# Performance work log

Measured on AMD Instinct MI355X. Metric: run time of the kernel, lower is better.

The kernel has to match this reference:

```python
import jax, jax.numpy as jnp
import numpy as np

B, H = 1024, 256
HP = H // 2  # hyperparams_dim
W_SCALE = 0.08  # kaiming-uniform-like magnitude to keep tanh unsaturated


def setup_inputs() -> dict:
    key = jax.random.key(0)
    ks = jax.random.split(key, 8)
    return {
        "h_0": jax.random.normal(ks[0], (B, 1, H), dtype=jnp.float32),
        "h_t": jax.random.normal(ks[1], (B, 1, H), dtype=jnp.float32),
        "msg": jax.random.normal(ks[2], (B, 1, H), dtype=jnp.float32),
        "c": jax.random.uniform(ks[3], (1,), dtype=jnp.float32),
        "fc1_w": jax.random.normal(ks[4], (HP, H), dtype=jnp.float32) * W_SCALE,
        "fc2_w": jax.random.normal(ks[5], (HP, HP), dtype=jnp.float32) * W_SCALE,
        "fc3_w": jax.random.normal(ks[6], (HP, HP), dtype=jnp.float32) * W_SCALE,
        "fc4_w": jax.random.normal(ks[7], (2 * H * H, HP), dtype=jnp.float32) * W_SCALE,
    }


def reference(h_0, h_t, msg, c, fc1_w, fc2_w, fc3_w, fc4_w):
    # torch code clamps self.c into [0, 1] before use
    cc = jnp.clip(c, 0.0, 1.0)
    h = cc * h_0 + (1.0 - cc) * h_t                     # [B, 1, H]
    x = jnp.tanh(jnp.einsum('bsh,ph->bsp', h, fc1_w))    # [B, 1, HP]
    x = jnp.tanh(jnp.einsum('bsp,qp->bsq', x, fc2_w))    # [B, 1, HP]
    x = jnp.tanh(jnp.einsum('bsq,rq->bsr', x, fc3_w))    # [B, 1, HP]
    f4 = jnp.einsum('bsr,wr->bsw', x, fc4_w)             # [B, 1, 2*H*H]
    g1 = f4[..., : H * H].reshape(-1, H, H)              # [B, H, H]
    g2 = f4[..., H * H :].reshape(-1, H, H)              # [B, H, H]
    # F.linear(msg[i], g) == msg[i] @ g.T, batched over B
    g1_out = jnp.tanh(jnp.einsum('bsh,bkh->bsk', msg, g1))  # [B, 1, H]
    out = jnp.einsum('bsk,bok->bso', g1_out, g2)             # [B, 1, H]
    return out
```

## Files before the change

kernel.cpp:

```cpp
#include <hip/hip_runtime.h>
#include <hip/hip_bf16.h>

#define HDIM 256
#define HPDIM 128

typedef short bf8 __attribute__((ext_vector_type(8)));
typedef float f32x4 __attribute__((ext_vector_type(4)));

__device__ inline unsigned pkbf2(float a, float b) {
  float2 f; f.x = a; f.y = b;
  __hip_bfloat162 h = __float22bfloat162_rn(f);
  unsigned u; __builtin_memcpy(&u, &h, 4); return u;
}
__device__ inline unsigned short bfbits(float v) {
  __hip_bfloat16 h = __float2bfloat16(v);
  unsigned short u; __builtin_memcpy(&u, &h, 2); return u;
}
__device__ inline uint4 pack8u(float4 a, float4 b) {
  uint4 r;
  r.x = pkbf2(a.x, a.y); r.y = pkbf2(a.z, a.w);
  r.z = pkbf2(b.x, b.y); r.w = pkbf2(b.z, b.w);
  return r;
}
__device__ inline float fast_tanh(float x) {
  float t = __expf(2.0f * x);
  return 1.0f - 2.0f * __builtin_amdgcn_rcpf(t + 1.0f);
}
__device__ inline bf8 wfrag(const float* __restrict__ s) {
  float4 a = *(const float4*)s, b = *(const float4*)(s + 4);
  uint4 u = pack8u(a, b);
  bf8 r; __builtin_memcpy(&r, &u, 16); return r;
}

__global__ __launch_bounds__(256) void k_prep(
    const float* __restrict__ h0, const float* __restrict__ htv,
    const float* __restrict__ cp,
    const float* __restrict__ w1, const float* __restrict__ w2,
    const float* __restrict__ w3, const float* __restrict__ msg,
    short* __restrict__ x3f, float* __restrict__ msgTT) {
  const int t = threadIdx.x;
  const int bx = blockIdx.x;

  if (bx >= 64) {
    const int b0 = (bx - 64) * 64;
    #pragma unroll
    for (int it = 0; it < 16; ++it) {
      int u = it * 256 + t;
      int bl = u & 63, g = u >> 6;
      float4 v = *(const float4*)(msg + (size_t)(b0 + bl) * HDIM + g * 4);
      *(float4*)(msgTT + (size_t)g * 4096 + (b0 + bl) * 4) = v;
    }
    return;
  }

  __shared__ char hbuf[8192];
  __shared__ char xa[4096];
  __shared__ char xb[4096];
  const int wave = t >> 6, lane = t & 63;
  const int r16 = lane & 15, quad = lane >> 4;
  const int b0 = bx * 16;
  const float cc = fminf(fmaxf(cp[0], 0.f), 1.f);

  #pragma unroll
  for (int it = 0; it < 2; ++it) {
    int flat = it * 2048 + t * 8;
    int row = flat >> 8, col = flat & 255, kb = col >> 3;
    int gi = (b0 + row) * HDIM + col;
    float4 a = *(const float4*)(h0 + gi);
    float4 b = *(const float4*)(htv + gi);
    float4 va, vb;
    va.x = cc*a.x + (1.f-cc)*b.x; va.y = cc*a.y + (1.f-cc)*b.y;
    va.z = cc*a.z + (1.f-cc)*b.z; va.w = cc*a.w + (1.f-cc)*b.w;
    a = *(const float4*)(h0 + gi + 4); b = *(const float4*)(htv + gi + 4);
    vb.x = cc*a.x + (1.f-cc)*b.x; vb.y = cc*a.y + (1.f-cc)*b.y;
    vb.z = cc*a.z + (1.f-cc)*b.z; vb.w = cc*a.w + (1.f-cc)*b.w;
    *(uint4*)(hbuf + row*512 + ((kb ^ (row & 7)) << 4)) = pack8u(va, vb);
  }
  __syncthreads();

  {
    f32x4 acc[2] = {};
    #pragma unroll
    for (int ks = 0; ks < 8; ++ks) {
      bf8 af = *(bf8*)(hbuf + r16*512 + (((ks*4 + quad) ^ (r16 & 7)) << 4));
      #pragma unroll
      for (int nt = 0; nt < 2; ++nt) {
        bf8 bw_ = wfrag(w1 + ((wave*2 + nt)*16 + r16) * 256 + ks*32 + quad*8);
        acc[nt] = __builtin_amdgcn_mfma_f32_16x16x32_bf16(af, bw_, acc[nt], 0, 0, 0);
      }
    }
    #pragma unroll
    for (int nt = 0; nt < 2; ++nt)
      #pragma unroll
      for (int i = 0; i < 4; ++i) {
        int row = quad*4 + i, col = wave*32 + nt*16 + r16;
        *(unsigned short*)(xa + row*256 + (((col >> 3) ^ (row & 7)) << 4) + ((col & 7) << 1))
            = bfbits(fast_tanh(acc[nt][i]));
      }
  }
  __syncthreads();
  {
    f32x4 acc[2] = {};
    #pragma unroll
    for (int ks = 0; ks < 4; ++ks) {
      bf8 af = *(bf8*)(xa + r16*256 + (((ks*4 + quad) ^ (r16 & 7)) << 4));
      #pragma unroll
      for (int nt = 0; nt < 2; ++nt) {
        bf8 bw_ = wfrag(w2 + ((wave*2 + nt)*16 + r16) * 128 + ks*32 + quad*8);
        acc[nt] = __builtin_amdgcn_mfma_f32_16x16x32_bf16(af, bw_, acc[nt], 0, 0, 0);
      }
    }
    #pragma unroll
    for (int nt = 0; nt < 2; ++nt)
      #pragma unroll
      for (int i = 0; i < 4; ++i) {
        int row = quad*4 + i, col = wave*32 + nt*16 + r16;
        *(unsigned short*)(xb + row*256 + (((col >> 3) ^ (row & 7)) << 4) + ((col & 7) << 1))
            = bfbits(fast_tanh(acc[nt][i]));
      }
  }
  __syncthreads();
  {
    f32x4 acc[2] = {};
    #pragma unroll
    for (int ks = 0; ks < 4; ++ks) {
      bf8 af = *(bf8*)(xb + r16*256 + (((ks*4 + quad) ^ (r16 & 7)) << 4));
      #pragma unroll
      for (int nt = 0; nt < 2; ++nt) {
        bf8 bw_ = wfrag(w3 + ((wave*2 + nt)*16 + r16) * 128 + ks*32 + quad*8);
        acc[nt] = __builtin_amdgcn_mfma_f32_16x16x32_bf16(af, bw_, acc[nt], 0, 0, 0);
      }
    }
    #pragma unroll
    for (int nt = 0; nt < 2; ++nt)
      #pragma unroll
      for (int i = 0; i < 4; ++i) {
        int row = quad*4 + i, col = wave*32 + nt*16 + r16;
        *(unsigned short*)(xa + row*256 + (((col >> 3) ^ (row & 7)) << 4) + ((col & 7) << 1))
            = bfbits(fast_tanh(acc[nt][i]));
      }
  }
  __syncthreads();
  {
    int ks = t >> 6, l = t & 63, q2 = l >> 4, rr = l & 15;
    uint4 d = *(uint4*)(xa + rr*256 + (((ks*4 + q2) ^ (rr & 7)) << 4));
    *(uint4*)(x3f + (size_t)((bx*4 + ks)*64 + l)*8) = d;
  }
}

template<int PHASE>
__global__ __launch_bounds__(1024, 4) void k_hyper(
    const short* __restrict__ x3f, const float* __restrict__ wTT,
    const float* __restrict__ fc4, float* __restrict__ outp) {
  __shared__ char lds[65536];
  const int bxs = blockIdx.x;
  const int kcol = ((bxs & 7) << 5) | (bxs >> 3);
  const int t = threadIdx.x, wave = t >> 6, lane = t & 63;
  const int r16 = lane & 15, quad = lane >> 4;
  const int bw = wave * 64;

  bf8 xf[4][4];
  #pragma unroll
  for (int nt = 0; nt < 4; ++nt)
    #pragma unroll
    for (int ks = 0; ks < 4; ++ks)
      xf[nt][ks] = *(const bf8*)(x3f +
          (size_t)(((wave*4 + nt)*4 + ks)*64 + lane)*8);
  #pragma unroll
  for (int nt = 0; nt < 4; ++nt)
    #pragma unroll
    for (int ks = 0; ks < 4; ++ks)
      asm volatile("" : "+v"(xf[nt][ks]));

  const float* src = fc4 + ((size_t)(PHASE ? 65536 : 0) + (size_t)kcol * 256) * HPDIM;
  #pragma unroll
  for (int it = 0; it < 4; ++it) {
    int cidx = it * 1024 + t;
    int row = cidx >> 4, kb = cidx & 15;
    const float* s = src + cidx * 8;
    float4 a = *(const float4*)s, b = *(const float4*)(s + 4);
    *(uint4*)(lds + row*256 + ((kb ^ (row & 7)) << 4)) = pack8u(a, b);
  }
  __syncthreads();

  float gacc[4] = {0.f, 0.f, 0.f, 0.f};
  const float* wbase = wTT + (size_t)quad * 4096 + (bw + r16) * 4;

  #pragma unroll 1
  for (int hg = 0; hg < 16; ++hg) {
    float4 wv[4];
    #pragma unroll
    for (int nt = 0; nt < 4; ++nt)
      wv[nt] = *(const float4*)(wbase + (size_t)hg*16384 + nt*64);
    const int row = hg*16 + r16;
    bf8 af[4];
    #pragma unroll
    for (int ks = 0; ks < 4; ++ks)
      af[ks] = *(bf8*)(lds + row*256 + (((ks*4 + quad) ^ (row & 7)) << 4));
    #pragma unroll
    for (int nt = 0; nt < 4; ++nt) {
      f32x4 acc = {};
      #pragma unroll
      for (int ks = 0; ks < 4; ++ks)
        acc = __builtin_amdgcn_mfma_f32_16x16x32_bf16(af[ks], xf[nt][ks], acc, 0, 0, 0);
      gacc[nt] += acc[0]*wv[nt].x + acc[1]*wv[nt].y + acc[2]*wv[nt].z + acc[3]*wv[nt].w;
    }
  }

  #pragma unroll
  for (int nt = 0; nt < 4; ++nt) {
    float v = gacc[nt];
    v += __shfl_xor(v, 16);
    v += __shfl_xor(v, 32);
    if (quad == 0) {
      int b = bw + nt*16 + r16;
      if (PHASE == 0) outp[(size_t)(kcol >> 2)*4096 + b*4 + (kcol & 3)] = fast_tanh(v);
      else            outp[b*HDIM + kcol] = v;
    }
  }
}

extern "C" void kernel_launch(void* const* d_in, const int* in_sizes, int n_in,
                              void* d_out, int out_size, void* d_ws, size_t ws_size,
                              hipStream_t stream) {
  const float* h0  = (const float*)d_in[0];
  const float* htt = (const float*)d_in[1];
  const float* msg = (const float*)d_in[2];
  const float* c   = (const float*)d_in[3];
  const float* w1  = (const float*)d_in[4];
  const float* w2  = (const float*)d_in[5];
  const float* w3  = (const float*)d_in[6];
  const float* w4  = (const float*)d_in[7];
  float* out = (float*)d_out;

  short* x3f  = (short*)d_ws;
  float* g1TT = (float*)((char*)d_ws + 262144);
  float* msgTT= (float*)((char*)d_ws + 262144 + 1048576);

  k_prep<<<dim3(80), dim3(256), 0, stream>>>(h0, htt, c, w1, w2, w3, msg,
                                             x3f, msgTT);
  k_hyper<0><<<dim3(256), dim3(1024), 0, stream>>>(x3f, msgTT, w4, g1TT);
  k_hyper<1><<<dim3(256), dim3(1024), 0, stream>>>(x3f, g1TT, w4, out);
}
```

Measured before the change: 155.5 us.

## Tile hyper kernel over two output columns and half the batch per block

Each k_hyper block now converts and caches two fc4 column slices (128 KB of LDS) instead of one, and covers half of the batch instead of all of it. Every wave processes 32 batch rows against both slices, so each x3/w fragment load feeds twice as many MFMAs. The fc4 slices are now loaded twice across the grid, once per batch half. The larger LDS footprint cuts occupancy to one block per CU, which may weaken latency hiding.

```diff
diff --git a/kernel.cpp b/kernel.cpp
--- a/kernel.cpp
+++ b/kernel.cpp
@@ -152,72 +152,85 @@
 __global__ __launch_bounds__(1024, 4) void k_hyper(
     const short* __restrict__ x3f, const float* __restrict__ wTT,
     const float* __restrict__ fc4, float* __restrict__ outp) {
-  __shared__ char lds[65536];
+  __shared__ char lds[131072];
   const int bxs = blockIdx.x;
-  const int kcol = ((bxs & 7) << 5) | (bxs >> 3);
+  const int xcd = bxs & 7, idx = bxs >> 3;
+  const int half = idx & 1;
+  const int pair = xcd * 16 + (idx >> 1);
+  const int kbase = pair * 2;
   const int t = threadIdx.x, wave = t >> 6, lane = t & 63;
   const int r16 = lane & 15, quad = lane >> 4;
-  const int bw = wave * 64;
-
-  bf8 xf[4][4];
-  #pragma unroll
-  for (int nt = 0; nt < 4; ++nt)
+  const int bw = half * 512 + wave * 32;
+
+  bf8 xf[2][4];
+  #pragma unroll
+  for (int nt = 0; nt < 2; ++nt) {
+    int g = half*32 + wave*2 + nt;
     #pragma unroll
     for (int ks = 0; ks < 4; ++ks)
-      xf[nt][ks] = *(const bf8*)(x3f +
-          (size_t)(((wave*4 + nt)*4 + ks)*64 + lane)*8);
-  #pragma unroll
-  for (int nt = 0; nt < 4; ++nt)
+      xf[nt][ks] = *(const bf8*)(x3f + (size_t)((g*4 + ks)*64 + lane)*8);
+  }
+  #pragma unroll
+  for (int nt = 0; nt < 2; ++nt)
     #pragma unroll
     for (int ks = 0; ks < 4; ++ks)
       asm volatile("" : "+v"(xf[nt][ks]));
 
-  const float* src = fc4 + ((size_t)(PHASE ? 65536 : 0) + (size_t)kcol * 256) * HPDIM;
-  #pragma unroll
-  for (int it = 0; it < 4; ++it) {
+  const float* src = fc4 + ((size_t)(PHASE ? 65536 : 0) + (size_t)kbase * 256) * HPDIM;
+  #pragma unroll
+  for (int it = 0; it < 8; ++it) {
     int cidx = it * 1024 + t;
-    int row = cidx >> 4, kb = cidx & 15;
-    const float* s = src + cidx * 8;
-    float4 a = *(const float4*)s, b = *(const float4*)(s + 4);
-    *(uint4*)(lds + row*256 + ((kb ^ (row & 7)) << 4)) = pack8u(a, b);
-  }
-  __syncthreads();
-
-  float gacc[4] = {0.f, 0.f, 0.f, 0.f};
+    int s = cidx >> 12, c2 = cidx & 4095;
+    int row = c2 >> 4, kb = c2 & 15;
+    const float* sp = src + cidx * 8;
+    float4 a = *(const float4*)sp, b = *(const float4*)(sp + 4);
+    *(uint4*)(lds + s*65536 + row*256 + ((kb ^ (row & 7)) << 4)) = pack8u(a, b);
+  }
+  __syncthreads();
+
+  float gacc[2][2] = {{0.f, 0.f}, {0.f, 0.f}};
   const float* wbase = wTT + (size_t)quad * 4096 + (bw + r16) * 4;
 
   #pragma unroll 1
   for (int hg = 0; hg < 16; ++hg) {
-    float4 wv[4];
-    #pragma unroll
-    for (int nt = 0; nt < 4; ++nt)
+    float4 wv[2];
+    #pragma unroll
+    for (int nt = 0; nt < 2; ++nt)
       wv[nt] = *(const float4*)(wbase + (size_t)hg*16384 + nt*64);
     const int row = hg*16 + r16;
-    bf8 af[4];
-    #pragma unroll
-    for (int ks = 0; ks < 4; ++ks)
-      af[ks] = *(bf8*)(lds + row*256 + (((ks*4 + quad) ^ (row & 7)) << 4));
-    #pragma unroll
-    for (int nt = 0; nt < 4; ++nt) {
-      f32x4 acc = {};
-      #pragma unroll
-      for (int ks = 0; ks < 4; ++ks)
-        acc = __builtin_amdgcn_mfma_f32_16x16x32_bf16(af[ks], xf[nt][ks], acc, 0, 0, 0);
-      gacc[nt] += acc[0]*wv[nt].x + acc[1]*wv[nt].y + acc[2]*wv[nt].z + acc[3]*wv[nt].w;
-    }
-  }
-
-  #pragma unroll
-  for (int nt = 0; nt < 4; ++nt) {
-    float v = gacc[nt];
-    v += __shfl_xor(v, 16);
-    v += __shfl_xor(v, 32);
-    if (quad == 0) {
-      int b = bw + nt*16 + r16;
-      if (PHASE == 0) outp[(size_t)(kcol >> 2)*4096 + b*4 + (kcol & 3)] = fast_tanh(v);
-      else            outp[b*HDIM + kcol] = v;
-    }
-  }
+    bf8 af0[4], af1[4];
+    #pragma unroll
+    for (int ks = 0; ks < 4; ++ks) {
+      af0[ks] = *(bf8*)(lds +         row*256 + (((ks*4 + quad) ^ (row & 7)) << 4));
+      af1[ks] = *(bf8*)(lds + 65536 + row*256 + (((ks*4 + quad) ^ (row & 7)) << 4));
+    }
+    #pragma unroll
+    for (int nt = 0; nt < 2; ++nt) {
+      f32x4 a0 = {}, a1 = {};
+      #pragma unroll
+      for (int ks = 0; ks < 4; ++ks) {
+        a0 = __builtin_amdgcn_mfma_f32_16x16x32_bf16(af0[ks], xf[nt][ks], a0, 0, 0, 0);
+        a1 = __builtin_amdgcn_mfma_f32_16x16x32_bf16(af1[ks], xf[nt][ks], a1, 0, 0, 0);
+      }
+      gacc[0][nt] += a0[0]*wv[nt].x + a0[1]*wv[nt].y + a0[2]*wv[nt].z + a0[3]*wv[nt].w;
+      gacc[1][nt] += a1[0]*wv[nt].x + a1[1]*wv[nt].y + a1[2]*wv[nt].z + a1[3]*wv[nt].w;
+    }
+  }
+
+  #pragma unroll
+  for (int s = 0; s < 2; ++s)
+    #pragma unroll
+    for (int nt = 0; nt < 2; ++nt) {
+      float v = gacc[s][nt];
+      v += __shfl_xor(v, 16);
+      v += __shfl_xor(v, 32);
+      if (quad == 0) {
+        int b = bw + nt*16 + r16;
+        int kcol = kbase + s;
+        if (PHASE == 0) outp[(size_t)(kcol >> 2)*4096 + b*4 + (kcol & 3)] = fast_tanh(v);
+        else            outp[b*HDIM + kcol] = v;
+      }
+    }
 }
 
 extern "C" void kernel_launch(void* const* d_in, const int* in_sizes, int n_in,
```

New measurement: 152.5 us. No clear change (-1.9%).

## Stream fc4 slab into LDS via async global_load_lds triple-buffered ring

Applied to the files above, without the earlier changes.

Replaces the direct register-staged load and bf16 conversion of each block's fc4 slab with asynchronous global-to-LDS loads of 16 KB chunks into a three-slot ring. Each chunk is then read from the ring, converted to bf16 and written into the swizzled slab. The aim is to overlap global memory latency with the conversion and to cut register pressure during the prologue. It adds 48 KB of LDS per block, which can lower occupancy, and introduces eight barriers in the load phase.

```diff
diff --git a/kernel.cpp b/kernel.cpp
--- a/kernel.cpp
+++ b/kernel.cpp
@@ -30,6 +30,12 @@
   float4 a = *(const float4*)s, b = *(const float4*)(s + 4);
   uint4 u = pack8u(a, b);
   bf8 r; __builtin_memcpy(&r, &u, 16); return r;
+}
+
+typedef const __attribute__((address_space(1))) unsigned int* gas_ptr;
+typedef __attribute__((address_space(3))) unsigned int* las_ptr;
+__device__ inline void gld_lds16(const void* g, void* l) {
+  __builtin_amdgcn_global_load_lds((gas_ptr)g, (las_ptr)l, 16, 0, 0);
 }
 
 __global__ __launch_bounds__(256) void k_prep(
@@ -152,13 +158,19 @@
 __global__ __launch_bounds__(1024, 4) void k_hyper(
     const short* __restrict__ x3f, const float* __restrict__ wTT,
     const float* __restrict__ fc4, float* __restrict__ outp) {
-  __shared__ char lds[65536];
+  __shared__ char lds[65536 + 49152];
+  char* slab = lds;
+  char* ring = lds + 65536;
   const int bxs = blockIdx.x;
   const int kcol = ((bxs & 7) << 5) | (bxs >> 3);
   const int t = threadIdx.x, wave = t >> 6, lane = t & 63;
   const int r16 = lane & 15, quad = lane >> 4;
   const int bw = wave * 64;
 
+  const float* src = fc4 + ((size_t)(PHASE ? 65536 : 0) + (size_t)kcol * 256) * HPDIM;
+
+  gld_lds16(src + t * 4, ring + t * 16);
+
   bf8 xf[4][4];
   #pragma unroll
   for (int nt = 0; nt < 4; ++nt)
@@ -172,14 +184,20 @@
     for (int ks = 0; ks < 4; ++ks)
       asm volatile("" : "+v"(xf[nt][ks]));
 
-  const float* src = fc4 + ((size_t)(PHASE ? 65536 : 0) + (size_t)kcol * 256) * HPDIM;
-  #pragma unroll
-  for (int it = 0; it < 4; ++it) {
-    int cidx = it * 1024 + t;
-    int row = cidx >> 4, kb = cidx & 15;
-    const float* s = src + cidx * 8;
-    float4 a = *(const float4*)s, b = *(const float4*)(s + 4);
-    *(uint4*)(lds + row*256 + ((kb ^ (row & 7)) << 4)) = pack8u(a, b);
+  #pragma unroll
+  for (int c = 0; c < 8; ++c) {
+    if (c < 7)
+      gld_lds16(src + (c + 1) * 4096 + t * 4, ring + ((c + 1) % 3) * 16384 + t * 16);
+    if (c < 7) asm volatile("s_waitcnt vmcnt(1) lgkmcnt(0)" ::: "memory");
+    else       asm volatile("s_waitcnt vmcnt(0) lgkmcnt(0)" ::: "memory");
+    __builtin_amdgcn_s_barrier();
+    __builtin_amdgcn_sched_barrier(0);
+    {
+      f32x4 v = *(const f32x4*)(ring + (c % 3) * 16384 + t * 16);
+      int row = c * 32 + (t >> 5), kb = (t & 31) >> 1;
+      uint2 o; o.x = pkbf2(v[0], v[1]); o.y = pkbf2(v[2], v[3]);
+      *(uint2*)(slab + row * 256 + ((kb ^ (row & 7)) << 4) + (t & 1) * 8) = o;
+    }
   }
   __syncthreads();
 
@@ -196,7 +214,7 @@
     bf8 af[4];
     #pragma unroll
     for (int ks = 0; ks < 4; ++ks)
-      af[ks] = *(bf8*)(lds + row*256 + (((ks*4 + quad) ^ (row & 7)) << 4));
+      af[ks] = *(bf8*)(slab + row*256 + (((ks*4 + quad) ^ (row & 7)) << 4));
     #pragma unroll
     for (int nt = 0; nt < 4; ++nt) {
       f32x4 acc = {};
```

Measured after the change: 155.6 us. Within noise of the previous version (+0.1%).
